# Performance work log

Hardware: AMD Instinct MI355X
Metric: run time of the kernel (lower is better)

Reference implementation:

```python
import jax, jax.numpy as jnp
import numpy as np

CHUNK = 128
EPS = 1e-12


def causal_prod(q, k, v, chunk=CHUNK):
    """Chunk-parallel causal linear attention numerator and denominator.
    q,k: [B,H,S,D]; v: [B,H,S,E].
    Returns N: [B,H,S,E] = q_n . cumsum_{m<=n}(k_m v_m^T)
            D: [B,H,S]   = q_n . cumsum_{m<=n} k_m
    """
    B, H, S, D = q.shape
    E = v.shape[-1]
    nc = S // chunk
    # [nc, B, H, C, D]
    qc = q.reshape(B, H, nc, chunk, D).transpose(2, 0, 1, 3, 4)
    kc = k.reshape(B, H, nc, chunk, D).transpose(2, 0, 1, 3, 4)
    vc = v.reshape(B, H, nc, chunk, E).transpose(2, 0, 1, 3, 4)
    mask = jnp.tril(jnp.ones((chunk, chunk), dtype=bool))  # j <= i

    def step(carry, xs):
        S_state, Z_state = carry  # [B,H,D,E], [B,H,D]
        qb, kb, vb = xs           # [B,H,C,D], [B,H,C,D], [B,H,C,E]
        scores = jnp.einsum('bhid,bhjd->bhij', qb, kb)
        scores = jnp.where(mask, scores, 0.0)
        # intra-chunk causal part + inter-chunk state part
        Nb = jnp.einsum('bhij,bhje->bhie', scores, vb) \
             + jnp.einsum('bhid,bhde->bhie', qb, S_state)
        Db = scores.sum(-1) + jnp.einsum('bhid,bhd->bhi', qb, Z_state)
        S_state = S_state + jnp.einsum('bhjd,bhje->bhde', kb, vb)
        Z_state = Z_state + kb.sum(axis=2)
        return (S_state, Z_state), (Nb, Db)

    init = (jnp.zeros((B, H, D, E), q.dtype), jnp.zeros((B, H, D), q.dtype))
    _, (N, Dv) = jax.lax.scan(step, init, (qc, kc, vc))
    N = N.transpose(1, 2, 0, 3, 4).reshape(B, H, S, E)
    Dv = Dv.transpose(1, 2, 0, 3).reshape(B, H, S)
    return N, Dv


def setup_inputs() -> dict:
    key = jax.random.key(0)
    k0, k1, k2, k3, k4 = jax.random.split(key, 5)
    B, H, S, D = 2, 8, 4096, 64
    # feature-mapped q/k are positive (softmax random features) -> uniform
    q = jax.random.uniform(k0, (B, H, S, D), dtype=jnp.float32)
    k = jax.random.uniform(k1, (B, H, S, D), dtype=jnp.float32)
    q_rot = jax.random.uniform(k2, (B, H, S, D), dtype=jnp.float32)
    k_rot = jax.random.uniform(k3, (B, H, S, D), dtype=jnp.float32)
    v = jax.random.normal(k4, (B, H, S, D), dtype=jnp.float32)
    return {"q": q, "k": k, "q_rot": q_rot, "k_rot": k_rot, "v": v, "horizon": 512}


def reference(q, k, q_rot, k_rot, v, horizon):
    # causal_linear_attention with local=horizon, rotary branch active
    N1, D1 = causal_prod(q, k, v)
    N2, D2 = causal_prod(q_rot, k_rot, v)
    N = N1 + N2
    Dd = D1 + D2
    local = horizon
    # subtract contribution of keys older than the local window
    ql = q[:, :, local:]
    kl = k[:, :, :-local]
    vl = v[:, :, :-local]
    qrl = q_rot[:, :, local:]
    krl = k_rot[:, :, :-local]
    Ns1, Ds1 = causal_prod(ql, kl, vl)
    Ns2, Ds2 = causal_prod(qrl, krl, vl)
    N = N.at[:, :, local:].add(-(Ns1 + Ns2))
    Dd = Dd.at[:, :, local:].add(-(Ds1 + Ds2))
    out = N * (1.0 / (Dd + EPS))[..., None]
    return out
```

## Files before the change

kernel.cpp:

```cpp
#include <hip/hip_runtime.h>

#define S_LEN 4096
#define Dh 64
#define THREADS 256
#define KC_TILE 16384
#define VT_TILE 8192
#define VT_BASE 16777216ull
#define WS_NEED 25165824ull

typedef __attribute__((ext_vector_type(8))) short bf16x8;
typedef __attribute__((ext_vector_type(4))) short bf16x4;
typedef __attribute__((ext_vector_type(4))) float f32x4;
typedef __attribute__((ext_vector_type(16))) float f32x16;
typedef __attribute__((ext_vector_type(4))) unsigned u32x4;

__device__ __forceinline__ short f2bf(float f) {
    union { float f; unsigned u; } c; c.f = f;
    unsigned u = c.u + 0x7FFFu + ((c.u >> 16) & 1u);
    return (short)(u >> 16);
}

__device__ __forceinline__ unsigned cvt_pk(float lo, float hi) {
    unsigned r;
    asm("v_cvt_pk_bf16_f32 %0, %1, %2" : "=v"(r) : "v"(lo), "v"(hi));
    return r;
}

__device__ __forceinline__ void pl32swap(unsigned& a, unsigned& b) {
    asm("v_permlane32_swap_b32 %0, %1" : "+v"(a), "+v"(b));
}

__device__ __forceinline__ void gload16(const void* g, void* l) {
    __builtin_amdgcn_global_load_lds(
        (const __attribute__((address_space(1))) unsigned int*)g,
        (__attribute__((address_space(3))) unsigned int*)l, 16, 0, 0);
}

__global__ __launch_bounds__(THREADS) void prepack(
    const float* __restrict__ k, const float* __restrict__ kr,
    const float* __restrict__ v, char* __restrict__ ws)
{
    const int t = blockIdx.x * THREADS + threadIdx.x;
    {
        const int bh = t >> 16;
        const int r1 = t & 65535;
        const int tile = r1 >> 10;
        const int r2 = r1 & 1023;
        const int row = r2 >> 4;
        const int f0 = (r2 & 15) * 8;
        const size_t rbase = ((size_t)bh * S_LEN + tile * 64 + row) * Dh;
        const float* src = (f0 < 64) ? (k + rbase + f0) : (kr + rbase + (f0 - 64));
        f32x4 a = *(const f32x4*)src;
        f32x4 b = *(const f32x4*)(src + 4);
        bf16x8 w;
        #pragma unroll
        for (int j = 0; j < 4; ++j) { w[j] = f2bf(a[j]); w[4 + j] = f2bf(b[j]); }
        const int off = row * 256 + ((f0 * 2) ^ ((row & 7) << 4));
        *(bf16x8*)(ws + (size_t)(bh * 64 + tile) * KC_TILE + off) = w;
    }
    {
        const int bh = t >> 16;
        const int r1 = t & 65535;
        const int tile = r1 >> 10;
        const int r2 = r1 & 1023;
        const int e = r2 & 63;
        const int k4 = r2 >> 6;
        const float* src = v + ((size_t)bh * S_LEN + tile * 64 + k4 * 4) * Dh + e;
        bf16x4 w;
        w[0] = f2bf(src[0]);
        w[1] = f2bf(src[Dh]);
        w[2] = f2bf(src[2 * Dh]);
        w[3] = f2bf(src[3 * Dh]);
        const int off = e * 128 + ((k4 * 8) ^ ((e & 7) << 4));
        *(bf16x4*)(ws + VT_BASE + (size_t)(bh * 64 + tile) * VT_TILE + off) = w;
    }
}

__global__ __launch_bounds__(THREADS, 2) void swin_attn3(
    const float* __restrict__ q, const float* __restrict__ qr,
    const char* __restrict__ ws, const int* __restrict__ hor,
    float* __restrict__ out)
{
    const int W = hor[0];
    const int bid = blockIdx.x;
    const int wg = (bid & 7) * 64 + (bid >> 3);
    const int bh = wg >> 5;
    const int q0 = (wg & 31) * 128;
    const size_t base = (size_t)bh * S_LEN * Dh;

    const int tid = threadIdx.x;
    const int lane = tid & 63;
    const int wv = tid >> 6;
    const int hi = lane >> 5;
    const int l32 = lane & 31;

    __shared__ __align__(16) char sK[2][KC_TILE];
    __shared__ __align__(16) char sV[2][VT_TILE];
    __shared__ float sD[4][32];

    const int qg = q0 + wv * 32 + l32;

    bf16x8 qf[8];
    {
        const float* qrow  = q  + base + (size_t)qg * Dh;
        const float* qrrow = qr + base + (size_t)qg * Dh;
        #pragma unroll
        for (int fs = 0; fs < 8; ++fs) {
            int feat = fs * 16 + hi * 8;
            const float* src = (feat < 64) ? (qrow + feat) : (qrrow + (feat - 64));
            f32x4 a = *(const f32x4*)src;
            f32x4 b = *(const f32x4*)(src + 4);
            bf16x8 fr;
            #pragma unroll
            for (int j = 0; j < 4; ++j) { fr[j] = f2bf(a[j]); fr[4 + j] = f2bf(b[j]); }
            qf[fs] = fr;
        }
    }

    f32x16 nacc0 = {};
    f32x16 nacc1 = {};
    float dsum = 0.f;

    const int lo_key = q0 - (W - 1);
    const int kt_lo = (lo_key <= 0) ? 0 : (lo_key >> 6);
    const int kt_hi = (q0 + 127) >> 6;

    const char* KcB = ws + (size_t)(bh << 6) * KC_TILE;
    const char* VtB = ws + VT_BASE + (size_t)(bh << 6) * VT_TILE;

    asm volatile("s_waitcnt vmcnt(0)" ::: "memory");
    __builtin_amdgcn_sched_barrier(0);

#define STAGE(B, KT)                                                              \
    do {                                                                          \
        const char* kg_ = KcB + (size_t)(KT) * KC_TILE + wv * 4096 + lane * 16;   \
        const char* vg_ = VtB + (size_t)(KT) * VT_TILE + wv * 2048 + lane * 16;   \
        _Pragma("unroll")                                                         \
        for (int i_ = 0; i_ < 4; ++i_)                                            \
            gload16(kg_ + i_ * 1024, &sK[B][wv * 4096 + i_ * 1024]);              \
        _Pragma("unroll")                                                         \
        for (int i_ = 0; i_ < 2; ++i_)                                            \
            gload16(vg_ + i_ * 1024, &sV[B][wv * 2048 + i_ * 1024]);              \
    } while (0)

    STAGE(0, kt_lo);

    int buf = 0;
    for (int kt = kt_lo; kt <= kt_hi; ++kt) {
        const int k0 = kt << 6;
        if (kt < kt_hi) {
            STAGE(buf ^ 1, kt + 1);
            asm volatile("s_waitcnt vmcnt(6)" ::: "memory");
        } else {
            asm volatile("s_waitcnt vmcnt(0)" ::: "memory");
        }
        __builtin_amdgcn_sched_barrier(0);
        __builtin_amdgcn_s_barrier();
        asm volatile("" ::: "memory");

        const char* Kb = sK[buf];
        const char* Vb = sV[buf];
        const bool dense = (k0 + 63 <= q0) && (k0 >= q0 + 128 - W);

        __builtin_amdgcn_s_setprio(1);

        f32x16 sac0 = {};
        f32x16 sac1 = {};
        const int krow0 = l32;
        const int krow1 = 32 + l32;
        const int sw0 = (krow0 & 7) << 4;
        #pragma unroll
        for (int fs = 0; fs < 8; ++fs) {
            const int fb = (fs * 16 + hi * 8) * 2;
            bf16x8 kf0 = *(const bf16x8*)(Kb + krow0 * 256 + (fb ^ sw0));
            bf16x8 kf1 = *(const bf16x8*)(Kb + krow1 * 256 + (fb ^ sw0));
            sac0 = __builtin_amdgcn_mfma_f32_32x32x16_bf16(kf0, qf[fs], sac0, 0, 0, 0);
            sac1 = __builtin_amdgcn_mfma_f32_32x32x16_bf16(kf1, qf[fs], sac1, 0, 0, 0);
        }

        #pragma unroll
        for (int kb = 0; kb < 2; ++kb) {
            f32x16 s = kb ? sac1 : sac0;
            if (!dense) {
                #pragma unroll
                for (int r = 0; r < 16; ++r) {
                    int key = k0 + kb * 32 + (r & 3) + 8 * (r >> 2) + 4 * hi;
                    if ((unsigned)(qg - key) >= (unsigned)W) s[r] = 0.f;
                }
            }
            #pragma unroll
            for (int r = 0; r < 16; ++r) dsum += s[r];

            unsigned w0 = cvt_pk(s[0],  s[1]);
            unsigned w1 = cvt_pk(s[2],  s[3]);
            unsigned w2 = cvt_pk(s[4],  s[5]);
            unsigned w3 = cvt_pk(s[6],  s[7]);
            unsigned w4 = cvt_pk(s[8],  s[9]);
            unsigned w5 = cvt_pk(s[10], s[11]);
            unsigned w6 = cvt_pk(s[12], s[13]);
            unsigned w7 = cvt_pk(s[14], s[15]);
            pl32swap(w0, w2);
            pl32swap(w1, w3);
            pl32swap(w4, w6);
            pl32swap(w5, w7);
            u32x4 p0v = {w0, w1, w2, w3};
            u32x4 p1v = {w4, w5, w6, w7};
            bf16x8 pa0 = __builtin_bit_cast(bf16x8, p0v);
            bf16x8 pa1 = __builtin_bit_cast(bf16x8, p1v);

            #pragma unroll
            for (int ks = 0; ks < 2; ++ks) {
                bf16x8 pa = ks ? pa1 : pa0;
                const int keyb = (kb * 32 + ks * 16 + hi * 8) * 2;
                const int e0 = l32;
                const int e1 = 32 + l32;
                const int swv = (l32 & 7) << 4;
                bf16x8 vf0 = *(const bf16x8*)(Vb + e0 * 128 + (keyb ^ swv));
                bf16x8 vf1 = *(const bf16x8*)(Vb + e1 * 128 + (keyb ^ swv));
                nacc0 = __builtin_amdgcn_mfma_f32_32x32x16_bf16(pa, vf0, nacc0, 0, 0, 0);
                nacc1 = __builtin_amdgcn_mfma_f32_32x32x16_bf16(pa, vf1, nacc1, 0, 0, 0);
            }
        }
        __builtin_amdgcn_s_setprio(0);

        asm volatile("" ::: "memory");
        __builtin_amdgcn_s_barrier();
        buf ^= 1;
    }
#undef STAGE

    unsigned da = __builtin_bit_cast(unsigned, dsum);
    unsigned db = da;
    pl32swap(da, db);
    float dfull = __builtin_bit_cast(float, da) + __builtin_bit_cast(float, db);
    float rcq = 1.0f / (dfull + 1e-12f);
    if (lane < 32) sD[wv][l32] = rcq;
    float rcv[16];
    #pragma unroll
    for (int r = 0; r < 16; ++r)
        rcv[r] = sD[wv][(r & 3) + 8 * (r >> 2) + 4 * hi];

    #pragma unroll
    for (int r = 0; r < 16; ++r) {
        const int qrow = q0 + wv * 32 + (r & 3) + 8 * (r >> 2) + 4 * hi;
        float* o = out + base + (size_t)qrow * Dh + l32;
        o[0]  = nacc0[r] * rcv[r];
        o[32] = nacc1[r] * rcv[r];
    }
}

__global__ __launch_bounds__(THREADS, 2) void swin_attn_fb(
    const float* __restrict__ q, const float* __restrict__ k,
    const float* __restrict__ qr, const float* __restrict__ kr,
    const float* __restrict__ v, const int* __restrict__ hor,
    float* __restrict__ out)
{
    const int W = hor[0];
    const int q0 = blockIdx.x * 128;
    const int bh = blockIdx.y;
    const size_t base = (size_t)bh * S_LEN * Dh;

    const int tid = threadIdx.x;
    const int lane = tid & 63;
    const int wv = tid >> 6;
    const int g = lane >> 4;
    const int l16 = lane & 15;

    __shared__ __align__(16) char sK[64 * 256];
    __shared__ __align__(16) char sV[64 * 128];
    __shared__ __align__(16) char sS[4][32 * 128];

    typedef __attribute__((ext_vector_type(4))) float f4;
    bf16x8 qf[2][4];
    #pragma unroll
    for (int rb = 0; rb < 2; ++rb) {
        int qg = q0 + wv * 32 + rb * 16 + l16;
        const float* qrow  = q  + base + (size_t)qg * Dh;
        const float* qrrow = qr + base + (size_t)qg * Dh;
        #pragma unroll
        for (int fb = 0; fb < 4; ++fb) {
            int feat = fb * 32 + g * 8;
            const float* src = (feat < 64) ? (qrow + feat) : (qrrow + (feat - 64));
            f4 a = *(const f4*)src;
            f4 b = *(const f4*)(src + 4);
            bf16x8 fr;
            #pragma unroll
            for (int j = 0; j < 4; ++j) { fr[j] = f2bf(a[j]); fr[4 + j] = f2bf(b[j]); }
            qf[rb][fb] = fr;
        }
    }

    f32x4 nacc[2][4];
    f32x4 dacc[2];
    #pragma unroll
    for (int rb = 0; rb < 2; ++rb) {
        dacc[rb] = (f32x4){0.f, 0.f, 0.f, 0.f};
        #pragma unroll
        for (int eb = 0; eb < 4; ++eb) nacc[rb][eb] = (f32x4){0.f, 0.f, 0.f, 0.f};
    }
    bf16x8 ones;
    #pragma unroll
    for (int j = 0; j < 8; ++j) ones[j] = (short)0x3F80;

    const int lo_key = q0 - (W - 1);
    const int kt_lo = (lo_key <= 0) ? 0 : (lo_key >> 6);
    const int kt_hi = (q0 + 127) >> 6;

    for (int kt = kt_lo; kt <= kt_hi; ++kt) {
        const int k0 = kt << 6;
        __syncthreads();
        #pragma unroll
        for (int i = 0; i < 4; ++i) {
            int c = tid + THREADS * i;
            int row = c >> 4;
            int f0 = (c & 15) * 8;
            const float* src = (f0 < 64) ? (k  + base + (size_t)(k0 + row) * Dh + f0)
                                         : (kr + base + (size_t)(k0 + row) * Dh + (f0 - 64));
            f4 a = *(const f4*)src;
            f4 b = *(const f4*)(src + 4);
            bf16x8 w8;
            #pragma unroll
            for (int j = 0; j < 4; ++j) { w8[j] = f2bf(a[j]); w8[4 + j] = f2bf(b[j]); }
            int off = row * 256 + ((f0 * 2) ^ ((row & 7) << 4));
            *(bf16x8*)(sK + off) = w8;
        }
        #pragma unroll
        for (int i = 0; i < 4; ++i) {
            int c = tid + THREADS * i;
            int e = c & 63;
            int k4 = c >> 6;
            const float* src = v + base + (size_t)(k0 + k4 * 4) * Dh + e;
            bf16x4 w4;
            w4[0] = f2bf(src[0]); w4[1] = f2bf(src[Dh]);
            w4[2] = f2bf(src[2 * Dh]); w4[3] = f2bf(src[3 * Dh]);
            int off = e * 128 + ((k4 * 8) ^ ((e & 7) << 4));
            *(bf16x4*)(sV + off) = w4;
        }
        __syncthreads();

        const bool dense = (k0 + 63 <= q0) && (k0 >= q0 + 128 - W);
        #pragma unroll
        for (int kb = 0; kb < 4; ++kb) {
            bf16x8 kf[4];
            const int key = kb * 16 + l16;
            const int rowoff = key * 256;
            const int sw = (key & 7) << 4;
            #pragma unroll
            for (int fb = 0; fb < 4; ++fb)
                kf[fb] = *(const bf16x8*)(sK + rowoff + ((fb * 64 + g * 16) ^ sw));
            #pragma unroll
            for (int rb = 0; rb < 2; ++rb) {
                f32x4 s = {0.f, 0.f, 0.f, 0.f};
                #pragma unroll
                for (int fb = 0; fb < 4; ++fb)
                    s = __builtin_amdgcn_mfma_f32_16x16x32_bf16(qf[rb][fb], kf[fb], s, 0, 0, 0);
                const int qrow0 = rb * 16 + g * 4;
                const int qg0 = q0 + wv * 32 + qrow0;
                const int mg = k0 + kb * 16 + l16;
                if (!dense) {
                    #pragma unroll
                    for (int r = 0; r < 4; ++r) {
                        unsigned d = (unsigned)(qg0 + r - mg);
                        if (d >= (unsigned)W) s[r] = 0.f;
                    }
                }
                #pragma unroll
                for (int r = 0; r < 4; ++r) {
                    int row = qrow0 + r;
                    int off = row * 128 + (((kb * 16 + l16) * 2) ^ ((row & 7) << 4));
                    *(short*)(sS[wv] + off) = f2bf(s[r]);
                }
            }
        }
        #pragma unroll
        for (int kb2 = 0; kb2 < 2; ++kb2) {
            bf16x8 af[2];
            #pragma unroll
            for (int rb = 0; rb < 2; ++rb) {
                int row = rb * 16 + l16;
                int off = row * 128 + ((kb2 * 64 + g * 16) ^ ((row & 7) << 4));
                af[rb] = *(const bf16x8*)(sS[wv] + off);
            }
            #pragma unroll
            for (int rb = 0; rb < 2; ++rb)
                dacc[rb] = __builtin_amdgcn_mfma_f32_16x16x32_bf16(af[rb], ones, dacc[rb], 0, 0, 0);
            #pragma unroll
            for (int eb = 0; eb < 4; ++eb) {
                int e = eb * 16 + l16;
                int off = e * 128 + ((kb2 * 64 + g * 16) ^ ((e & 7) << 4));
                bf16x8 bfr = *(const bf16x8*)(sV + off);
                #pragma unroll
                for (int rb = 0; rb < 2; ++rb)
                    nacc[rb][eb] = __builtin_amdgcn_mfma_f32_16x16x32_bf16(af[rb], bfr, nacc[rb][eb], 0, 0, 0);
            }
        }
    }

    #pragma unroll
    for (int rb = 0; rb < 2; ++rb) {
        f32x4 rc;
        #pragma unroll
        for (int r = 0; r < 4; ++r) rc[r] = 1.0f / (dacc[rb][r] + 1e-12f);
        const int qg0 = q0 + wv * 32 + rb * 16 + g * 4;
        #pragma unroll
        for (int eb = 0; eb < 4; ++eb) {
            #pragma unroll
            for (int r = 0; r < 4; ++r) {
                out[base + (size_t)(qg0 + r) * Dh + eb * 16 + l16] = nacc[rb][eb][r] * rc[r];
            }
        }
    }
}

extern "C" void kernel_launch(void* const* d_in, const int* in_sizes, int n_in,
                              void* d_out, int out_size, void* d_ws, size_t ws_size,
                              hipStream_t stream) {
    const float* q  = (const float*)d_in[0];
    const float* k  = (const float*)d_in[1];
    const float* qr = (const float*)d_in[2];
    const float* kr = (const float*)d_in[3];
    const float* v  = (const float*)d_in[4];
    const int* hor  = (const int*)d_in[5];
    float* out = (float*)d_out;
    const int BH = in_sizes[0] / (S_LEN * Dh);

    if (ws_size >= WS_NEED) {
        hipLaunchKernelGGL(prepack, dim3(4096), dim3(THREADS), 0, stream,
                           k, kr, v, (char*)d_ws);
        hipLaunchKernelGGL(swin_attn3, dim3((S_LEN / 128) * BH), dim3(THREADS), 0, stream,
                           q, qr, (const char*)d_ws, hor, out);
    } else {
        hipLaunchKernelGGL(swin_attn_fb, dim3(S_LEN / 128, BH), dim3(THREADS), 0, stream,
                           q, k, qr, kr, v, hor, out);
    }
}
```

Before: 45.95 us.

## Use single-wave blocks loading prepacked MFMA fragments directly into registers

The prepack kernel now writes K and V in a lane-ordered fragment layout so each lane can fetch its MFMA operands with contiguous 16-byte global loads. The attention kernel drops LDS staging and barriers, becoming a one-wavefront block per 32 queries that register-prefetches the next key tile. This removes LDS traffic and block-level synchronization and gives four times as many workgroups. In exchange, each key tile is re-read from L2 by four times as many blocks, and register pressure rises because 24 fragment registers are held per lane.

```diff
diff --git a/kernel.cpp b/kernel.cpp
--- a/kernel.cpp
+++ b/kernel.cpp
@@ -2,11 +2,8 @@
 
 #define S_LEN 4096
 #define Dh 64
-#define THREADS 256
 #define KC_TILE 16384
 #define VT_TILE 8192
-#define VT_BASE 16777216ull
-#define WS_NEED 25165824ull
 
 typedef __attribute__((ext_vector_type(8))) short bf16x8;
 typedef __attribute__((ext_vector_type(4))) short bf16x4;
@@ -30,75 +27,72 @@
     asm("v_permlane32_swap_b32 %0, %1" : "+v"(a), "+v"(b));
 }
 
-__device__ __forceinline__ void gload16(const void* g, void* l) {
-    __builtin_amdgcn_global_load_lds(
-        (const __attribute__((address_space(1))) unsigned int*)g,
-        (__attribute__((address_space(3))) unsigned int*)l, 16, 0, 0);
-}
-
-__global__ __launch_bounds__(THREADS) void prepack(
+__global__ __launch_bounds__(256) void prepack2(
     const float* __restrict__ k, const float* __restrict__ kr,
-    const float* __restrict__ v, char* __restrict__ ws)
+    const float* __restrict__ v, char* __restrict__ ws,
+    unsigned long long vt_base, int k_slots)
 {
-    const int t = blockIdx.x * THREADS + threadIdx.x;
-    {
+    const int t = blockIdx.x * 256 + threadIdx.x;
+    if (t < k_slots) {
         const int bh = t >> 16;
-        const int r1 = t & 65535;
-        const int tile = r1 >> 10;
-        const int r2 = r1 & 1023;
-        const int row = r2 >> 4;
-        const int f0 = (r2 & 15) * 8;
-        const size_t rbase = ((size_t)bh * S_LEN + tile * 64 + row) * Dh;
-        const float* src = (f0 < 64) ? (k + rbase + f0) : (kr + rbase + (f0 - 64));
+        const int r = t & 65535;
+        const int tile = r >> 10;
+        const int s = r & 1023;
+        const int l = s & 63;
+        const int c = s >> 6;
+        const int fs = c >> 1, half = c & 1;
+        const int key = half * 32 + (l & 31);
+        const int f0 = fs * 16 + (l >> 5) * 8;
+        const size_t row = ((size_t)bh * S_LEN + tile * 64 + key) * Dh;
+        const float* src = (f0 < 64) ? (k + row + f0) : (kr + row + f0 - 64);
         f32x4 a = *(const f32x4*)src;
         f32x4 b = *(const f32x4*)(src + 4);
-        bf16x8 w;
-        #pragma unroll
-        for (int j = 0; j < 4; ++j) { w[j] = f2bf(a[j]); w[4 + j] = f2bf(b[j]); }
-        const int off = row * 256 + ((f0 * 2) ^ ((row & 7) << 4));
-        *(bf16x8*)(ws + (size_t)(bh * 64 + tile) * KC_TILE + off) = w;
-    }
-    {
-        const int bh = t >> 16;
-        const int r1 = t & 65535;
-        const int tile = r1 >> 10;
-        const int r2 = r1 & 1023;
-        const int e = r2 & 63;
-        const int k4 = r2 >> 6;
-        const float* src = v + ((size_t)bh * S_LEN + tile * 64 + k4 * 4) * Dh + e;
-        bf16x4 w;
-        w[0] = f2bf(src[0]);
-        w[1] = f2bf(src[Dh]);
-        w[2] = f2bf(src[2 * Dh]);
-        w[3] = f2bf(src[3 * Dh]);
-        const int off = e * 128 + ((k4 * 8) ^ ((e & 7) << 4));
-        *(bf16x4*)(ws + VT_BASE + (size_t)(bh * 64 + tile) * VT_TILE + off) = w;
-    }
-}
-
-__global__ __launch_bounds__(THREADS, 2) void swin_attn3(
+        u32x4 w;
+        w[0] = cvt_pk(a[0], a[1]); w[1] = cvt_pk(a[2], a[3]);
+        w[2] = cvt_pk(b[0], b[1]); w[3] = cvt_pk(b[2], b[3]);
+        *(u32x4*)(ws + (size_t)(bh * 64 + tile) * KC_TILE + s * 16) = w;
+    } else {
+        const int t2 = t - k_slots;
+        const int bh = t2 >> 15;
+        const int r = t2 & 32767;
+        const int tile = r >> 9;
+        const int s = r & 511;
+        const int l = s & 63;
+        const int c = s >> 6;
+        const int kb = c >> 2, ks = (c >> 1) & 1, eh = c & 1;
+        const int e = eh * 32 + (l & 31);
+        const int key0 = kb * 32 + ks * 16 + (l >> 5) * 8;
+        const float* src = v + ((size_t)bh * S_LEN + tile * 64 + key0) * Dh + e;
+        float x0 = src[0],      x1 = src[Dh],     x2 = src[2 * Dh], x3 = src[3 * Dh];
+        float x4 = src[4 * Dh], x5 = src[5 * Dh], x6 = src[6 * Dh], x7 = src[7 * Dh];
+        u32x4 w;
+        w[0] = cvt_pk(x0, x1); w[1] = cvt_pk(x2, x3);
+        w[2] = cvt_pk(x4, x5); w[3] = cvt_pk(x6, x7);
+        *(u32x4*)(ws + vt_base + (size_t)(bh * 64 + tile) * VT_TILE + s * 16) = w;
+    }
+}
+
+__global__ __launch_bounds__(64, 2) void swin_attn4(
     const float* __restrict__ q, const float* __restrict__ qr,
-    const char* __restrict__ ws, const int* __restrict__ hor,
-    float* __restrict__ out)
+    const char* __restrict__ ws, unsigned long long vt_base,
+    const int* __restrict__ hor, float* __restrict__ out)
 {
     const int W = hor[0];
+    const int nwg = gridDim.x;
+    const int cpx = nwg >> 3;
     const int bid = blockIdx.x;
-    const int wg = (bid & 7) * 64 + (bid >> 3);
-    const int bh = wg >> 5;
-    const int q0 = (wg & 31) * 128;
+    const int wg = (bid & 7) * cpx + (bid >> 3);
+    const int bh = wg >> 7;
+    const int q0 = (wg & 127) * 32;
     const size_t base = (size_t)bh * S_LEN * Dh;
 
-    const int tid = threadIdx.x;
-    const int lane = tid & 63;
-    const int wv = tid >> 6;
+    const int lane = threadIdx.x;
     const int hi = lane >> 5;
     const int l32 = lane & 31;
 
-    __shared__ __align__(16) char sK[2][KC_TILE];
-    __shared__ __align__(16) char sV[2][VT_TILE];
-    __shared__ float sD[4][32];
-
-    const int qg = q0 + wv * 32 + l32;
+    __shared__ float sD[32];
+
+    const int qg = q0 + l32;
 
     bf16x8 qf[8];
     {
@@ -107,13 +101,13 @@
         #pragma unroll
         for (int fs = 0; fs < 8; ++fs) {
             int feat = fs * 16 + hi * 8;
-            const float* src = (feat < 64) ? (qrow + feat) : (qrrow + (feat - 64));
+            const float* src = (feat < 64) ? (qrow + feat) : (qrrow + feat - 64);
             f32x4 a = *(const f32x4*)src;
             f32x4 b = *(const f32x4*)(src + 4);
-            bf16x8 fr;
-            #pragma unroll
-            for (int j = 0; j < 4; ++j) { fr[j] = f2bf(a[j]); fr[4 + j] = f2bf(b[j]); }
-            qf[fs] = fr;
+            u32x4 w;
+            w[0] = cvt_pk(a[0], a[1]); w[1] = cvt_pk(a[2], a[3]);
+            w[2] = cvt_pk(b[0], b[1]); w[3] = cvt_pk(b[2], b[3]);
+            qf[fs] = __builtin_bit_cast(bf16x8, w);
         }
     }
 
@@ -123,59 +117,41 @@
 
     const int lo_key = q0 - (W - 1);
     const int kt_lo = (lo_key <= 0) ? 0 : (lo_key >> 6);
-    const int kt_hi = (q0 + 127) >> 6;
-
-    const char* KcB = ws + (size_t)(bh << 6) * KC_TILE;
-    const char* VtB = ws + VT_BASE + (size_t)(bh << 6) * VT_TILE;
-
-    asm volatile("s_waitcnt vmcnt(0)" ::: "memory");
-    __builtin_amdgcn_sched_barrier(0);
-
-#define STAGE(B, KT)                                                              \
-    do {                                                                          \
-        const char* kg_ = KcB + (size_t)(KT) * KC_TILE + wv * 4096 + lane * 16;   \
-        const char* vg_ = VtB + (size_t)(KT) * VT_TILE + wv * 2048 + lane * 16;   \
-        _Pragma("unroll")                                                         \
-        for (int i_ = 0; i_ < 4; ++i_)                                            \
-            gload16(kg_ + i_ * 1024, &sK[B][wv * 4096 + i_ * 1024]);              \
-        _Pragma("unroll")                                                         \
-        for (int i_ = 0; i_ < 2; ++i_)                                            \
-            gload16(vg_ + i_ * 1024, &sV[B][wv * 2048 + i_ * 1024]);              \
-    } while (0)
-
-    STAGE(0, kt_lo);
-
-    int buf = 0;
+    const int kt_hi = (q0 + 31) >> 6;
+
+    const char* Kc = ws + (size_t)(bh << 6) * KC_TILE + lane * 16;
+    const char* Vt = ws + vt_base + (size_t)(bh << 6) * VT_TILE + lane * 16;
+
+    bf16x8 kf[16];
+    bf16x8 vf[8];
+    {
+        const char* kp = Kc + (size_t)kt_lo * KC_TILE;
+        const char* vp = Vt + (size_t)kt_lo * VT_TILE;
+        #pragma unroll
+        for (int c = 0; c < 16; ++c) kf[c] = *(const bf16x8*)(kp + c * 1024);
+        #pragma unroll
+        for (int c = 0; c < 8; ++c)  vf[c] = *(const bf16x8*)(vp + c * 1024);
+    }
+
     for (int kt = kt_lo; kt <= kt_hi; ++kt) {
         const int k0 = kt << 6;
-        if (kt < kt_hi) {
-            STAGE(buf ^ 1, kt + 1);
-            asm volatile("s_waitcnt vmcnt(6)" ::: "memory");
-        } else {
-            asm volatile("s_waitcnt vmcnt(0)" ::: "memory");
-        }
-        __builtin_amdgcn_sched_barrier(0);
-        __builtin_amdgcn_s_barrier();
-        asm volatile("" ::: "memory");
-
-        const char* Kb = sK[buf];
-        const char* Vb = sV[buf];
-        const bool dense = (k0 + 63 <= q0) && (k0 >= q0 + 128 - W);
-
-        __builtin_amdgcn_s_setprio(1);
+        const int ktn = (kt < kt_hi) ? kt + 1 : kt_hi;
+        const bool dense = (k0 + 63 <= q0) && (k0 >= q0 + 32 - W);
 
         f32x16 sac0 = {};
         f32x16 sac1 = {};
-        const int krow0 = l32;
-        const int krow1 = 32 + l32;
-        const int sw0 = (krow0 & 7) << 4;
+        __builtin_amdgcn_s_setprio(1);
         #pragma unroll
         for (int fs = 0; fs < 8; ++fs) {
-            const int fb = (fs * 16 + hi * 8) * 2;
-            bf16x8 kf0 = *(const bf16x8*)(Kb + krow0 * 256 + (fb ^ sw0));
-            bf16x8 kf1 = *(const bf16x8*)(Kb + krow1 * 256 + (fb ^ sw0));
-            sac0 = __builtin_amdgcn_mfma_f32_32x32x16_bf16(kf0, qf[fs], sac0, 0, 0, 0);
-            sac1 = __builtin_amdgcn_mfma_f32_32x32x16_bf16(kf1, qf[fs], sac1, 0, 0, 0);
+            sac0 = __builtin_amdgcn_mfma_f32_32x32x16_bf16(kf[fs * 2],     qf[fs], sac0, 0, 0, 0);
+            sac1 = __builtin_amdgcn_mfma_f32_32x32x16_bf16(kf[fs * 2 + 1], qf[fs], sac1, 0, 0, 0);
+        }
+        __builtin_amdgcn_s_setprio(0);
+
+        {
+            const char* kp = Kc + (size_t)ktn * KC_TILE;
+            #pragma unroll
+            for (int c = 0; c < 16; ++c) kf[c] = *(const bf16x8*)(kp + c * 1024);
         }
 
         #pragma unroll
@@ -208,48 +184,45 @@
             bf16x8 pa0 = __builtin_bit_cast(bf16x8, p0v);
             bf16x8 pa1 = __builtin_bit_cast(bf16x8, p1v);
 
+            __builtin_amdgcn_s_setprio(1);
             #pragma unroll
             for (int ks = 0; ks < 2; ++ks) {
                 bf16x8 pa = ks ? pa1 : pa0;
-                const int keyb = (kb * 32 + ks * 16 + hi * 8) * 2;
-                const int e0 = l32;
-                const int e1 = 32 + l32;
-                const int swv = (l32 & 7) << 4;
-                bf16x8 vf0 = *(const bf16x8*)(Vb + e0 * 128 + (keyb ^ swv));
-                bf16x8 vf1 = *(const bf16x8*)(Vb + e1 * 128 + (keyb ^ swv));
-                nacc0 = __builtin_amdgcn_mfma_f32_32x32x16_bf16(pa, vf0, nacc0, 0, 0, 0);
-                nacc1 = __builtin_amdgcn_mfma_f32_32x32x16_bf16(pa, vf1, nacc1, 0, 0, 0);
-            }
-        }
-        __builtin_amdgcn_s_setprio(0);
-
-        asm volatile("" ::: "memory");
-        __builtin_amdgcn_s_barrier();
-        buf ^= 1;
-    }
-#undef STAGE
+                nacc0 = __builtin_amdgcn_mfma_f32_32x32x16_bf16(pa, vf[kb * 4 + ks * 2],     nacc0, 0, 0, 0);
+                nacc1 = __builtin_amdgcn_mfma_f32_32x32x16_bf16(pa, vf[kb * 4 + ks * 2 + 1], nacc1, 0, 0, 0);
+            }
+            __builtin_amdgcn_s_setprio(0);
+        }
+
+        {
+            const char* vp = Vt + (size_t)ktn * VT_TILE;
+            #pragma unroll
+            for (int c = 0; c < 8; ++c) vf[c] = *(const bf16x8*)(vp + c * 1024);
+        }
+    }
 
     unsigned da = __builtin_bit_cast(unsigned, dsum);
     unsigned db = da;
     pl32swap(da, db);
     float dfull = __builtin_bit_cast(float, da) + __builtin_bit_cast(float, db);
     float rcq = 1.0f / (dfull + 1e-12f);
-    if (lane < 32) sD[wv][l32] = rcq;
+    if (lane < 32) sD[l32] = rcq;
+    __syncthreads();
     float rcv[16];
     #pragma unroll
     for (int r = 0; r < 16; ++r)
-        rcv[r] = sD[wv][(r & 3) + 8 * (r >> 2) + 4 * hi];
+        rcv[r] = sD[(r & 3) + 8 * (r >> 2) + 4 * hi];
 
     #pragma unroll
     for (int r = 0; r < 16; ++r) {
-        const int qrow = q0 + wv * 32 + (r & 3) + 8 * (r >> 2) + 4 * hi;
+        const int qrow = q0 + (r & 3) + 8 * (r >> 2) + 4 * hi;
         float* o = out + base + (size_t)qrow * Dh + l32;
         o[0]  = nacc0[r] * rcv[r];
         o[32] = nacc1[r] * rcv[r];
     }
 }
 
-__global__ __launch_bounds__(THREADS, 2) void swin_attn_fb(
+__global__ __launch_bounds__(256, 2) void swin_attn_fb(
     const float* __restrict__ q, const float* __restrict__ k,
     const float* __restrict__ qr, const float* __restrict__ kr,
     const float* __restrict__ v, const int* __restrict__ hor,
@@ -270,7 +243,6 @@
     __shared__ __align__(16) char sV[64 * 128];
     __shared__ __align__(16) char sS[4][32 * 128];
 
-    typedef __attribute__((ext_vector_type(4))) float f4;
     bf16x8 qf[2][4];
     #pragma unroll
     for (int rb = 0; rb < 2; ++rb) {
@@ -281,8 +253,8 @@
         for (int fb = 0; fb < 4; ++fb) {
             int feat = fb * 32 + g * 8;
             const float* src = (feat < 64) ? (qrow + feat) : (qrrow + (feat - 64));
-            f4 a = *(const f4*)src;
-            f4 b = *(const f4*)(src + 4);
+            f32x4 a = *(const f32x4*)src;
+            f32x4 b = *(const f32x4*)(src + 4);
             bf16x8 fr;
             #pragma unroll
             for (int j = 0; j < 4; ++j) { fr[j] = f2bf(a[j]); fr[4 + j] = f2bf(b[j]); }
@@ -311,13 +283,13 @@
         __syncthreads();
         #pragma unroll
         for (int i = 0; i < 4; ++i) {
-            int c = tid + THREADS * i;
+            int c = tid + 256 * i;
             int row = c >> 4;
             int f0 = (c & 15) * 8;
             const float* src = (f0 < 64) ? (k  + base + (size_t)(k0 + row) * Dh + f0)
                                          : (kr + base + (size_t)(k0 + row) * Dh + (f0 - 64));
-            f4 a = *(const f4*)src;
-            f4 b = *(const f4*)(src + 4);
+            f32x4 a = *(const f32x4*)src;
+            f32x4 b = *(const f32x4*)(src + 4);
             bf16x8 w8;
             #pragma unroll
             for (int j = 0; j < 4; ++j) { w8[j] = f2bf(a[j]); w8[4 + j] = f2bf(b[j]); }
@@ -326,7 +298,7 @@
         }
         #pragma unroll
         for (int i = 0; i < 4; ++i) {
-            int c = tid + THREADS * i;
+            int c = tid + 256 * i;
             int e = c & 63;
             int k4 = c >> 6;
             const float* src = v + base + (size_t)(k0 + k4 * 4) * Dh + e;
@@ -422,15 +394,20 @@
     const float* v  = (const float*)d_in[4];
     const int* hor  = (const int*)d_in[5];
     float* out = (float*)d_out;
+
     const int BH = in_sizes[0] / (S_LEN * Dh);
-
-    if (ws_size >= WS_NEED) {
-        hipLaunchKernelGGL(prepack, dim3(4096), dim3(THREADS), 0, stream,
-                           k, kr, v, (char*)d_ws);
-        hipLaunchKernelGGL(swin_attn3, dim3((S_LEN / 128) * BH), dim3(THREADS), 0, stream,
-                           q, qr, (const char*)d_ws, hor, out);
+    const unsigned long long vt_base = (unsigned long long)BH * 64 * KC_TILE;
+    const unsigned long long ws_need = (unsigned long long)BH * 64 * (KC_TILE + VT_TILE);
+    const int k_slots = BH * 65536;
+
+    if (ws_size >= ws_need) {
+        const int total_slots = BH * (65536 + 32768);
+        hipLaunchKernelGGL(prepack2, dim3(total_slots / 256), dim3(256), 0, stream,
+                           k, kr, v, (char*)d_ws, vt_base, k_slots);
+        hipLaunchKernelGGL(swin_attn4, dim3(BH * 128), dim3(64), 0, stream,
+                           q, qr, (const char*)d_ws, vt_base, hor, out);
     } else {
-        hipLaunchKernelGGL(swin_attn_fb, dim3(S_LEN / 128, BH), dim3(THREADS), 0, stream,
+        hipLaunchKernelGGL(swin_attn_fb, dim3(S_LEN / 128, BH), dim3(256), 0, stream,
                            q, k, qr, kr, v, hor, out);
     }
 }
```

New measurement: 42.31 us. -7.9%, faster.
